# Optimization experiments

Measured on AMD Instinct MI355X. Metric: run time of the kernel, lower is better.

## Reference

```python
import jax, jax.numpy as jnp
import numpy as np

N_AGENTS = 32
N_HEADS = 8
HEAD_DIM = 32          # atten_dim // n_heads
HID = 256              # rnn_hidden_dim
ATT = 256              # atten_dim
N_ACT = 32
NEG = -1e9             # finite stand-in for -inf; exp underflows to 0 in softmax


def setup_inputs() -> dict:
    key = jax.random.key(0)
    ks = jax.random.split(key, 20)
    B, N, E = 4096, 64, 128
    w = lambda k, shape: (jax.random.normal(k, shape, jnp.float32) * 0.05)
    return {
        "inputs": jax.random.normal(ks[0], (B, N, E), jnp.float32),
        "hidden_state": jax.random.normal(ks[1], (B, N_AGENTS, HID), jnp.float32) * 0.1,
        "fc1_w": w(ks[2], (HID, E)), "fc1_b": jnp.zeros((HID,), jnp.float32),
        "q_w": w(ks[3], (ATT, HID)), "q_b": jnp.zeros((ATT,), jnp.float32),
        "k_w": w(ks[4], (ATT, HID)), "k_b": jnp.zeros((ATT,), jnp.float32),
        "v_w": w(ks[5], (ATT, HID)), "v_b": jnp.zeros((ATT,), jnp.float32),
        "w_ih": w(ks[6], (3 * HID, ATT)), "w_hh": w(ks[7], (3 * HID, HID)),
        "b_ih": jnp.zeros((3 * HID,), jnp.float32), "b_hh": jnp.zeros((3 * HID,), jnp.float32),
        "out_w": w(ks[8], (N_ACT, HID)), "out_b": jnp.zeros((N_ACT,), jnp.float32),
        "obs_mask": jax.random.randint(ks[9], (B, N, N), 0, 2).astype(bool),
        "scenario_mask": jax.random.randint(ks[10], (B, N_AGENTS), 0, 2).astype(bool),
    }


def reference(inputs, hidden_state, fc1_w, fc1_b, q_w, q_b, k_w, k_b, v_w, v_b,
              w_ih, w_hh, b_ih, b_hh, out_w, out_b, obs_mask, scenario_mask):
    B, N, _ = inputs.shape
    A, nh, e = N_AGENTS, N_HEADS, HEAD_DIM
    # fc1 + ReLU: [B, N, HID]
    x = jax.nn.relu(inputs @ fc1_w.T + fc1_b)
    # multi-head projections; queries only for the first A entities (agents)
    q = (x[:, :A] @ q_w.T + q_b).reshape(B, A, nh, e).transpose(0, 2, 1, 3)   # [B,nh,A,e]
    k = (x @ k_w.T + k_b).reshape(B, N, nh, e).transpose(0, 2, 3, 1)          # [B,nh,e,N]
    v = jax.nn.relu(x @ v_w.T + v_b).reshape(B, N, nh, e).transpose(0, 2, 1, 3)  # [B,nh,N,e]
    score = jnp.einsum('bhae,bhen->bhan', q, k) / np.float32(np.sqrt(e))      # [B,nh,A,N]
    m = obs_mask[:, :A, :][:, None, :, :]                                      # [B,1,A,N]
    score = jnp.where(m, NEG, score)
    w = jax.nn.softmax(score, axis=-1)
    # original: fully-masked rows give NaN then are zeroed; here zero all masked slots
    w = jnp.where(m, 0.0, w)
    att = jnp.einsum('bhan,bhne->bhae', w, v)                                  # [B,nh,A,e]
    att = att.transpose(0, 2, 1, 3).reshape(B * A, nh * e)                     # [B*A, ATT]
    # GRUCell step (PyTorch gate ordering: r, z, n)
    h0 = hidden_state.reshape(B * A, HID)
    gi = att @ w_ih.T + b_ih
    gh = h0 @ w_hh.T + b_hh
    ir, iz, in_ = jnp.split(gi, 3, axis=-1)
    hr, hz, hn = jnp.split(gh, 3, axis=-1)
    r = jax.nn.sigmoid(ir + hr)
    z = jax.nn.sigmoid(iz + hz)
    n = jnp.tanh(in_ + r * hn)
    h = (1.0 - z) * n + z * h0
    h = h.reshape(B, A, HID)
    am = scenario_mask[:, :, None]                                             # [B,A,1]
    h = jnp.where(am, 0.0, h)
    q_out = h @ out_w.T + out_b
    q_out = jnp.where(am, 0.0, q_out)
    return q_out, h
```

## Files before the change

kernel.cpp:

```cpp
#include <hip/hip_runtime.h>


using bfrag = __attribute__((ext_vector_type(8))) short;
using ffrag = __attribute__((ext_vector_type(4))) float;

#define MFMA(a,b,c) __builtin_amdgcn_mfma_f32_16x16x32_bf16((a),(b),(c),0,0,0)
#define SWZ(row,col,S,xm) ((row)*(S) + ((((col)&~7) ^ (((row)&(xm))<<3)) | ((col)&7)))

#define OFF_A2   0L
#define OFF_FC1  67108864L
#define OFF_QW   67141632L
#define OFF_KW   67207168L
#define OFF_VW   67272704L
#define OFF_WIH  67338240L
#define OFF_WHH  67534848L
#define OFF_OW   67731456L
#define OFF_FLAG 67739648L
#define WS_NEED_BYTES 135479552L

__device__ inline unsigned short f2bf(float x){
  union { float f; unsigned u; } v; v.f = x;
  unsigned r = v.u + 0x7fffu + ((v.u >> 16) & 1u);
  return (unsigned short)(r >> 16);
}
__device__ inline float bf2f(short b){
  union { unsigned u; float f; } v; v.u = ((unsigned)(unsigned short)b) << 16;
  return v.f;
}
__device__ inline bool getmask(const void* p, long i, int byteflag){
  return byteflag ? (((const unsigned char*)p)[i] != 0)
                  : (((const int*)p)[i] != 0);
}
__device__ inline ffrag fzero(){ ffrag z; z[0]=0.f; z[1]=0.f; z[2]=0.f; z[3]=0.f; return z; }
__device__ inline void gload16(const short* g, short* l){
  __builtin_amdgcn_global_load_lds((const __attribute__((address_space(1))) void*)g,
                                   (__attribute__((address_space(3))) void*)l, 16, 0, 0);
}

__global__ void k0_prep(const float* __restrict__ fc1, const float* __restrict__ qw,
    const float* __restrict__ kw, const float* __restrict__ vw, const float* __restrict__ wih,
    const float* __restrict__ whh, const float* __restrict__ ow, const float* __restrict__ h0,
    const void* __restrict__ obsm, short* __restrict__ ws){
  long tid = (long)blockIdx.x*blockDim.x + threadIdx.x;
  long n = (long)gridDim.x*blockDim.x;
  if (tid == 0){
    const int* mi = (const int*)obsm;
    int f = 0;
    for (int i=0;i<256;i++){ if ((unsigned)mi[i] > 1u){ f = 1; break; } }
    ((int*)(ws + OFF_FLAG))[0] = f;
  }
  for (long i=tid; i<32768; i+=n) ws[OFF_FC1+i] = (short)f2bf(fc1[i]);
  for (long i=tid; i<65536; i+=n){
    ws[OFF_QW+i] = (short)f2bf(qw[i]);
    ws[OFF_KW+i] = (short)f2bf(kw[i]);
    ws[OFF_VW+i] = (short)f2bf(vw[i]);
  }
  for (long i=tid; i<196608; i+=n){
    int R = (int)(i >> 8), c = (int)(i & 255);
    int gate = R >> 8, grow = R & 255;
    int jb = grow >> 5, row = grow & 31;
    long dst = (long)((jb*3 + gate)*32 + row)*256 + (c ^ ((row&7)<<3));
    ws[OFF_WIH + dst] = (short)f2bf(wih[i]);
    ws[OFF_WHH + dst] = (short)f2bf(whh[i]);
  }
  for (long i=tid; i<8192; i+=n) ws[OFF_OW+i] = (short)f2bf(ow[i]);
  const float2* h2 = (const float2*)h0;
  unsigned* a2u = (unsigned*)(ws + OFF_A2);
  for (long i=tid; i<16777216L; i+=n){
    long row = i >> 7; int j = (int)(i & 127);
    float2 v = h2[i];
    unsigned pk = (unsigned)f2bf(v.x) | ((unsigned)f2bf(v.y) << 16);
    a2u[row*256 + 128 + j] = pk;
  }
}

__global__ __launch_bounds__(512) void k1_fqkv(const float* __restrict__ inp,
    const short* __restrict__ fc1B, const float* __restrict__ fc1_b,
    const short* __restrict__ wq, const short* __restrict__ wk, const short* __restrict__ wv,
    const float* __restrict__ qb, const float* __restrict__ kb, const float* __restrict__ vb,
    short* __restrict__ A2, short* __restrict__ kC, short* __restrict__ vC, int chunkB){
  __shared__ __align__(16) short smem[65536];
  short* a_s  = smem;
  short* fw_s = smem + 16384;
  short* x_s  = smem;
  int t = threadIdx.x;
  long R0 = (long)blockIdx.x * 128;
  long grow0 = (long)chunkB*131072 + R0;
  int lane = t&63, w = t>>6, lr = lane&15, ko = lane>>4;
  for (int i=0;i<4;i++){
    int c = t + i*512; int row = c>>4; int cc = (c&15)*8;
    const float* src = inp + (grow0 + row)*128 + cc;
    float4 f0 = *(const float4*)src; float4 f1 = *(const float4*)(src+4);
    bfrag v8;
    v8[0]=(short)f2bf(f0.x); v8[1]=(short)f2bf(f0.y); v8[2]=(short)f2bf(f0.z); v8[3]=(short)f2bf(f0.w);
    v8[4]=(short)f2bf(f1.x); v8[5]=(short)f2bf(f1.y); v8[6]=(short)f2bf(f1.z); v8[7]=(short)f2bf(f1.w);
    *(bfrag*)(a_s + SWZ(row, cc, 128, 7)) = v8;
  }
  for (int i=0;i<8;i++){
    int c = t + i*512; int row = c>>4; int cc = (c&15)*8;
    *(bfrag*)(fw_s + SWZ(row, cc, 128, 7)) = *(const bfrag*)(fc1B + row*128 + cc);
  }
  __syncthreads();
  ffrag acc1[16];
  #pragma unroll
  for (int i=0;i<16;i++) acc1[i]=fzero();
  for (int ks=0; ks<4; ks++){
    int kc = ks*32 + ko*8;
    bfrag a = *(const bfrag*)(a_s + SWZ(w*16+lr, kc, 128, 7));
    #pragma unroll
    for (int nt=0; nt<16; nt++){
      bfrag bb = *(const bfrag*)(fw_s + SWZ(nt*16+lr, kc, 128, 7));
      acc1[nt] = MFMA(a, bb, acc1[nt]);
    }
  }
  __syncthreads();
  #pragma unroll
  for (int nt=0; nt<16; nt++){
    float bias = fc1_b[nt*16+lr];
    #pragma unroll
    for (int r=0;r<4;r++){
      int row = w*16 + ko*4 + r;
      float v = acc1[nt][r] + bias; v = v>0.f?v:0.f;
      x_s[SWZ(row, nt*16+lr, 256, 7)] = (short)f2bf(v);
    }
  }
  bfrag a_r[8];
  #pragma unroll
  for (int ks=0; ks<8; ks++)
    a_r[ks] = *(const bfrag*)(x_s + SWZ(w*16+lr, ks*32+ko*8, 256, 7));
  auto STAGE2 = [&](int s){
    int kind = s>>2; int rb = (s&3)*64;
    const short* wsrc = (kind==0?wq:(kind==1?wk:wv)) + (long)rb*256;
    short* dst = smem + 32768 + (s&1)*16384;
    #pragma unroll
    for (int i=0;i<4;i++){
      int c = t + i*512; int row = c>>5; int cc = (c&31)*8;
      *(bfrag*)(dst + SWZ(row, cc, 256, 7)) = *(const bfrag*)(wsrc + (long)row*256 + cc);
    }
  };
  STAGE2(0);
  __syncthreads();
  for (int s=0; s<12; s++){
    if (s < 11) STAGE2(s+1);
    const short* wcur = smem + 32768 + (s&1)*16384;
    ffrag acc2[4];
    #pragma unroll
    for (int i=0;i<4;i++) acc2[i]=fzero();
    #pragma unroll
    for (int ks=0; ks<8; ks++){
      int kc = ks*32 + ko*8;
      #pragma unroll
      for (int nt=0; nt<4; nt++){
        bfrag bb = *(const bfrag*)(wcur + SWZ(nt*16+lr, kc, 256, 7));
        acc2[nt] = MFMA(a_r[ks], bb, acc2[nt]);
      }
    }
    int kind = s>>2; int rb = (s&3)*64;
    const float* bsrc = (kind==0?qb:(kind==1?kb:vb));
    #pragma unroll
    for (int nt=0; nt<4; nt++){
      int colk = rb + nt*16 + lr;
      float bias = bsrc[colk];
      #pragma unroll
      for (int r=0;r<4;r++){
        int row = w*16 + ko*4 + r;
        long rl = R0 + row;
        float v = acc2[nt][r] + bias;
        if (kind==0){
          if ((row&32)==0){
            long grow = grow0 + row;
            long qrow = ((grow>>6)<<5) + (grow&31);
            A2[qrow*512 + colk] = (short)f2bf(v);
          }
        } else if (kind==1){
          kC[rl*256 + colk] = (short)f2bf(v);
        } else {
          v = v>0.f?v:0.f;
          vC[rl*256 + colk] = (short)f2bf(v);
        }
      }
    }
    __syncthreads();
  }
}

__global__ __launch_bounds__(512,4) void k2_attn(const short* __restrict__ kC,
    const short* __restrict__ vC, const void* __restrict__ obsm, short* __restrict__ A2,
    const int* __restrict__ flagp, int chunkB){
  __shared__ __align__(16) short vT_s[8][2048];
  __shared__ __align__(16) short p_s[8][2048];
  __shared__ unsigned char m_s[2048];
  int t = threadIdx.x, bl = blockIdx.x;
  long b = (long)chunkB*2048 + bl;
  int lane = t&63, w = t>>6, lr = lane&15, ko = lane>>4;
  int mflag = *flagp;
  if (mflag){
    uchar4 mv = *(const uchar4*)((const unsigned char*)obsm + b*4096 + t*4);
    m_s[t*4]=mv.x; m_s[t*4+1]=mv.y; m_s[t*4+2]=mv.z; m_s[t*4+3]=mv.w;
  } else {
    int4 mv = *(const int4*)((const int*)obsm + b*4096 + t*4);
    m_s[t*4]  =(unsigned char)(mv.x!=0); m_s[t*4+1]=(unsigned char)(mv.y!=0);
    m_s[t*4+2]=(unsigned char)(mv.z!=0); m_s[t*4+3]=(unsigned char)(mv.w!=0);
  }
  const int h = w;
  const short* qh = A2 + ((long)b*32)*512 + h*32 + ko*8;
  bfrag a_q[2];
  #pragma unroll
  for (int mt=0; mt<2; mt++) a_q[mt] = *(const bfrag*)(qh + (long)(mt*16+lr)*512);
  const short* kh = kC + ((long)bl*64)*256 + h*32 + ko*8;
  bfrag b_k[4];
  #pragma unroll
  for (int nt=0; nt<4; nt++) b_k[nt] = *(const bfrag*)(kh + (nt*16+lr)*256);
  #pragma unroll
  for (int i=0;i<4;i++){
    int n = i*16 + (lane>>2); int e0 = (lane&3)*8;
    bfrag vv = *(const bfrag*)(vC + ((long)bl*64 + n)*256 + h*32 + e0);
    #pragma unroll
    for (int j=0;j<8;j++) vT_s[w][SWZ(e0+j, n, 64, 7)] = vv[j];
  }
  ffrag sc[2][4];
  #pragma unroll
  for (int mt=0; mt<2; mt++)
    #pragma unroll
    for (int nt=0; nt<4; nt++) sc[mt][nt] = MFMA(a_q[mt], b_k[nt], fzero());
  __syncthreads();
  const float scale = 0.17677669529663687f;
  float rsi[2][4];
  #pragma unroll
  for (int mt=0; mt<2; mt++){
    #pragma unroll
    for (int r=0; r<4; r++){
      int arow = mt*16 + ko*4 + r;
      float sv[4]; int mk[4];
      #pragma unroll
      for (int nt=0; nt<4; nt++){
        mk[nt] = m_s[arow*64 + nt*16 + lr];
        sv[nt] = sc[mt][nt][r] * scale;
      }
      float mx = -3.0e38f;
      #pragma unroll
      for (int nt=0; nt<4; nt++) if (!mk[nt]) mx = fmaxf(mx, sv[nt]);
      for (int d=1; d<16; d<<=1) mx = fmaxf(mx, __shfl_xor(mx, d));
      float sum = 0.f;
      #pragma unroll
      for (int nt=0; nt<4; nt++){
        float p = mk[nt] ? 0.f : __expf(sv[nt]-mx);
        sv[nt] = p; sum += p;
      }
      for (int d=1; d<16; d<<=1) sum += __shfl_xor(sum, d);
      rsi[mt][r] = sum > 0.f ? 1.f/sum : 0.f;
      #pragma unroll
      for (int nt=0; nt<4; nt++)
        p_s[w][SWZ(arow, nt*16+lr, 64, 7)] = (short)f2bf(sv[nt]);
    }
  }
  ffrag o[2][2];
  #pragma unroll
  for (int mt=0;mt<2;mt++)
    #pragma unroll
    for (int nt=0;nt<2;nt++) o[mt][nt]=fzero();
  #pragma unroll
  for (int kk=0; kk<2; kk++){
    int kc = kk*32 + ko*8;
    bfrag pa0 = *(const bfrag*)(p_s[w]  + SWZ(lr,    kc, 64, 7));
    bfrag pa1 = *(const bfrag*)(p_s[w]  + SWZ(16+lr, kc, 64, 7));
    bfrag bv0 = *(const bfrag*)(vT_s[w] + SWZ(lr,    kc, 64, 7));
    bfrag bv1 = *(const bfrag*)(vT_s[w] + SWZ(16+lr, kc, 64, 7));
    o[0][0]=MFMA(pa0,bv0,o[0][0]); o[0][1]=MFMA(pa0,bv1,o[0][1]);
    o[1][0]=MFMA(pa1,bv0,o[1][0]); o[1][1]=MFMA(pa1,bv1,o[1][1]);
  }
  #pragma unroll
  for (int mt=0; mt<2; mt++)
    #pragma unroll
    for (int nt=0; nt<2; nt++)
      #pragma unroll
      for (int r=0; r<4; r++){
        int a = mt*16 + ko*4 + r;
        A2[((long)b*32 + a)*512 + h*32 + nt*16 + lr] = (short)f2bf(o[mt][nt][r]*rsi[mt][r]);
      }
}

__global__ __launch_bounds__(512) void k3_gru(const short* __restrict__ A2,
    const short* __restrict__ wihS, const short* __restrict__ whhS,
    const float* __restrict__ b_ih, const float* __restrict__ b_hh,
    const void* __restrict__ scen, float* __restrict__ hout, const int* __restrict__ flagp){
  __shared__ __align__(16) short w_s[2][24576];
  int t = threadIdx.x, bid = blockIdx.x;
  long R0 = (long)bid * 128;
  int mflag = *flagp;
  int lane = t&63, w = t>>6, lr = lane&15, ko = lane>>4;
  long rowbase = R0 + (long)w*16;
  auto STAGE = [&](int jb, int part){
    const short* src = (part ? whhS : wihS) + (long)jb*24576;
    short* dst = w_s[part];
    #pragma unroll
    for (int i=0;i<6;i++)
      gload16(src + (long)(i*512 + t)*8, dst + (i*512 + (t & ~63))*8);
  };
  STAGE(0,0);
  const short* Ab = A2 + (rowbase + lr)*512 + ko*8;
  bfrag A[16];
  #pragma unroll
  for (int ks=0; ks<16; ks++)
    A[ks] = *(const bfrag*)(Ab + ks*32);
  __syncthreads();
  for (int jb=0; jb<8; jb++){
    ffrag aR[2], aZ[2], aI[2], aN[2];
    #pragma unroll
    for (int nt=0;nt<2;nt++){ aR[nt]=fzero(); aZ[nt]=fzero(); aI[nt]=fzero(); aN[nt]=fzero(); }
    STAGE(jb,1);
    {
      const short* wc = w_s[0];
      #pragma unroll
      for (int ks=0; ks<8; ks++){
        int kc = ks*32 + ko*8;
        #pragma unroll
        for (int nt=0; nt<2; nt++){
          bfrag bR = *(const bfrag*)(wc + 0*8192 + SWZ(nt*16+lr, kc, 256, 7));
          aR[nt] = MFMA(A[ks], bR, aR[nt]);
          bfrag bZ = *(const bfrag*)(wc + 1*8192 + SWZ(nt*16+lr, kc, 256, 7));
          aZ[nt] = MFMA(A[ks], bZ, aZ[nt]);
          bfrag bX = *(const bfrag*)(wc + 2*8192 + SWZ(nt*16+lr, kc, 256, 7));
          aI[nt] = MFMA(A[ks], bX, aI[nt]);
        }
      }
    }
    __syncthreads();
    if (jb < 7) STAGE(jb+1,0);
    {
      const short* wc = w_s[1];
      #pragma unroll
      for (int ks=0; ks<8; ks++){
        int kc = ks*32 + ko*8;
        #pragma unroll
        for (int nt=0; nt<2; nt++){
          bfrag bR = *(const bfrag*)(wc + 0*8192 + SWZ(nt*16+lr, kc, 256, 7));
          aR[nt] = MFMA(A[8+ks], bR, aR[nt]);
          bfrag bZ = *(const bfrag*)(wc + 1*8192 + SWZ(nt*16+lr, kc, 256, 7));
          aZ[nt] = MFMA(A[8+ks], bZ, aZ[nt]);
          bfrag bX = *(const bfrag*)(wc + 2*8192 + SWZ(nt*16+lr, kc, 256, 7));
          aN[nt] = MFMA(A[8+ks], bX, aN[nt]);
        }
      }
    }
    #pragma unroll
    for (int nt=0; nt<2; nt++){
      int j = jb*32 + nt*16 + lr;
      float bir = b_ih[j],     bhr = b_hh[j];
      float biz = b_ih[256+j], bhz = b_hh[256+j];
      float bin = b_ih[512+j], bhn = b_hh[512+j];
      #pragma unroll
      for (int rr=0; rr<4; rr++){
        long row = rowbase + ko*4 + rr;
        float rg = 1.f/(1.f + __expf(-(aR[nt][rr] + bir + bhr)));
        float zg = 1.f/(1.f + __expf(-(aZ[nt][rr] + biz + bhz)));
        float ag = aI[nt][rr] + bin + rg*(aN[nt][rr] + bhn);
        float ng = 2.f/(1.f + __expf(-2.f*ag)) - 1.f;
        float h0v = bf2f(A2[row*512 + 256 + j]);
        float hv = (1.f - zg)*ng + zg*h0v;
        if (getmask(scen, row, mflag)) hv = 0.f;
        hout[row*256 + j] = hv;
      }
    }
    __syncthreads();
  }
}

__global__ __launch_bounds__(512) void k4_out(const float* __restrict__ hout,
    const short* __restrict__ ow, const float* __restrict__ out_b,
    const void* __restrict__ scen, float* __restrict__ qout, const int* __restrict__ flagp){
  __shared__ __align__(16) short ow_s[32*256];
  int t = threadIdx.x; long R0 = (long)blockIdx.x * 256;
  int mflag = *flagp;
  for (int i=0;i<2;i++){
    int c = t + i*512; int row = c >> 5; int cc = (c & 31)*8;
    *(bfrag*)(ow_s + SWZ(row, cc, 256, 7)) = *(const bfrag*)(ow + row*256 + cc);
  }
  __syncthreads();
  int lane = t&63, w = t>>6, lr = lane&15, ko = lane>>4;
  ffrag acc[2][2];
  #pragma unroll
  for (int a=0;a<2;a++) for (int bq=0;bq<2;bq++) acc[a][bq]=fzero();
  for (int ks=0; ks<8; ks++){
    int kc = ks*32 + ko*8;
    #pragma unroll
    for (int mi=0; mi<2; mi++){
      long row = R0 + (w*2+mi)*16 + lr;
      const float* hp = hout + row*256 + kc;
      float4 f0 = *(const float4*)hp; float4 f1 = *(const float4*)(hp+4);
      bfrag a;
      a[0]=(short)f2bf(f0.x); a[1]=(short)f2bf(f0.y); a[2]=(short)f2bf(f0.z); a[3]=(short)f2bf(f0.w);
      a[4]=(short)f2bf(f1.x); a[5]=(short)f2bf(f1.y); a[6]=(short)f2bf(f1.z); a[7]=(short)f2bf(f1.w);
      #pragma unroll
      for (int nt=0; nt<2; nt++){
        bfrag bb = *(const bfrag*)(ow_s + SWZ(nt*16+lr, kc, 256, 7));
        acc[mi][nt] = MFMA(a, bb, acc[mi][nt]);
      }
    }
  }
  #pragma unroll
  for (int mi=0;mi<2;mi++)
    #pragma unroll
    for (int nt=0;nt<2;nt++){
      int col = nt*16 + lr;
      float ob = out_b[col];
      #pragma unroll
      for (int r=0;r<4;r++){
        long row = R0 + (w*2+mi)*16 + ko*4 + r;
        float qv = acc[mi][nt][r] + ob;
        if (getmask(scen, row, mflag)) qv = 0.f;
        qout[row*32 + col] = qv;
      }
    }
}

extern "C" void kernel_launch(void* const* d_in, const int* in_sizes, int n_in,
                              void* d_out, int out_size, void* d_ws, size_t ws_size,
                              hipStream_t stream){
  const float* inputs = (const float*)d_in[0];
  const float* hidden = (const float*)d_in[1];
  const float* fc1_w  = (const float*)d_in[2];
  const float* fc1_b  = (const float*)d_in[3];
  const float* q_w    = (const float*)d_in[4];
  const float* q_b    = (const float*)d_in[5];
  const float* k_w    = (const float*)d_in[6];
  const float* k_b    = (const float*)d_in[7];
  const float* v_w    = (const float*)d_in[8];
  const float* v_b    = (const float*)d_in[9];
  const float* w_ih   = (const float*)d_in[10];
  const float* w_hh   = (const float*)d_in[11];
  const float* b_ih   = (const float*)d_in[12];
  const float* b_hh   = (const float*)d_in[13];
  const float* out_w  = (const float*)d_in[14];
  const float* out_b  = (const float*)d_in[15];
  const void* obsm    = d_in[16];
  const void* scen    = d_in[17];
  (void)in_sizes; (void)n_in; (void)out_size;
  if ((long)ws_size < WS_NEED_BYTES) return;
  short* ws = (short*)d_ws;
  const int* flagp = (const int*)(ws + OFF_FLAG);
  float* qout = (float*)d_out;
  float* hout = qout + 4194304;
  short* kCs = (short*)hout;
  short* vCs = kCs + 33554432L;
  short* A2  = ws + OFF_A2;

  hipLaunchKernelGGL(k0_prep, dim3(2048), dim3(256), 0, stream,
      fc1_w, q_w, k_w, v_w, w_ih, w_hh, out_w, hidden, obsm, ws);
  for (int c=0; c<2; c++){
    hipLaunchKernelGGL(k1_fqkv, dim3(1024), dim3(512), 0, stream,
        inputs, ws + OFF_FC1, fc1_b, ws + OFF_QW, ws + OFF_KW, ws + OFF_VW,
        q_b, k_b, v_b, A2, kCs, vCs, c);
    hipLaunchKernelGGL(k2_attn, dim3(2048), dim3(512), 0, stream,
        kCs, vCs, obsm, A2, flagp, c);
  }
  hipLaunchKernelGGL(k3_gru, dim3(1024), dim3(512), 0, stream,
      A2, ws + OFF_WIH, ws + OFF_WHH, b_ih, b_hh, scen, hout, flagp);
  hipLaunchKernelGGL(k4_out, dim3(512), dim3(512), 0, stream,
      hout, ws + OFF_OW, out_b, scen, qout, flagp);
}
```

Baseline: 612.8 us.

## Restage GRU weights into 32 KB phases to shrink LDS and deepen pipelining

Measured after the change: 612.5 us. Within noise of the previous version (-0.0%).

```diff
diff --git a/kernel.cpp b/kernel.cpp
--- a/kernel.cpp
+++ b/kernel.cpp
@@ -12,8 +12,7 @@
 #define OFF_QW   67141632L
 #define OFF_KW   67207168L
 #define OFF_VW   67272704L
-#define OFF_WIH  67338240L
-#define OFF_WHH  67534848L
+#define OFF_W6   67338240L
 #define OFF_OW   67731456L
 #define OFF_FLAG 67739648L
 #define WS_NEED_BYTES 135479552L
@@ -56,12 +55,13 @@
     ws[OFF_VW+i] = (short)f2bf(vw[i]);
   }
   for (long i=tid; i<196608; i+=n){
-    int R = (int)(i >> 8), c = (int)(i & 255);
-    int gate = R >> 8, grow = R & 255;
+    int gate = (int)(i >> 16);
+    int grow = (int)((i >> 8) & 255);
+    int c = (int)(i & 255);
     int jb = grow >> 5, row = grow & 31;
-    long dst = (long)((jb*3 + gate)*32 + row)*256 + (c ^ ((row&7)<<3));
-    ws[OFF_WIH + dst] = (short)f2bf(wih[i]);
-    ws[OFF_WHH + dst] = (short)f2bf(whh[i]);
+    int cs = c ^ ((row&7)<<3);
+    ws[OFF_W6 + ((long)((jb*6 + gate)*32 + row))*256 + cs]     = (short)f2bf(wih[i]);
+    ws[OFF_W6 + ((long)((jb*6 + 3 + gate)*32 + row))*256 + cs] = (short)f2bf(whh[i]);
   }
   for (long i=tid; i<8192; i+=n) ws[OFF_OW+i] = (short)f2bf(ow[i]);
   const float2* h2 = (const float2*)h0;
@@ -281,23 +281,22 @@
 }
 
 __global__ __launch_bounds__(512) void k3_gru(const short* __restrict__ A2,
-    const short* __restrict__ wihS, const short* __restrict__ whhS,
-    const float* __restrict__ b_ih, const float* __restrict__ b_hh,
+    const short* __restrict__ w6, const float* __restrict__ b_ih, const float* __restrict__ b_hh,
     const void* __restrict__ scen, float* __restrict__ hout, const int* __restrict__ flagp){
-  __shared__ __align__(16) short w_s[2][24576];
+  __shared__ __align__(16) short w_s[2][16384];
   int t = threadIdx.x, bid = blockIdx.x;
   long R0 = (long)bid * 128;
   int mflag = *flagp;
   int lane = t&63, w = t>>6, lr = lane&15, ko = lane>>4;
   long rowbase = R0 + (long)w*16;
-  auto STAGE = [&](int jb, int part){
-    const short* src = (part ? whhS : wihS) + (long)jb*24576;
-    short* dst = w_s[part];
-    #pragma unroll
-    for (int i=0;i<6;i++)
+  auto STAGE = [&](int ph){
+    const short* src = w6 + (long)ph*16384;
+    short* dst = w_s[ph&1];
+    #pragma unroll
+    for (int i=0;i<4;i++)
       gload16(src + (long)(i*512 + t)*8, dst + (i*512 + (t & ~63))*8);
   };
-  STAGE(0,0);
+  STAGE(0);
   const short* Ab = A2 + (rowbase + lr)*512 + ko*8;
   bfrag A[16];
   #pragma unroll
@@ -308,61 +307,53 @@
     ffrag aR[2], aZ[2], aI[2], aN[2];
     #pragma unroll
     for (int nt=0;nt<2;nt++){ aR[nt]=fzero(); aZ[nt]=fzero(); aI[nt]=fzero(); aN[nt]=fzero(); }
-    STAGE(jb,1);
-    {
-      const short* wc = w_s[0];
+    #pragma unroll
+    for (int p=0; p<3; p++){
+      int ph = jb*3 + p;
+      if (ph < 23) STAGE(ph+1);
+      const short* wc = w_s[ph&1];
       #pragma unroll
       for (int ks=0; ks<8; ks++){
         int kc = ks*32 + ko*8;
         #pragma unroll
         for (int nt=0; nt<2; nt++){
-          bfrag bR = *(const bfrag*)(wc + 0*8192 + SWZ(nt*16+lr, kc, 256, 7));
-          aR[nt] = MFMA(A[ks], bR, aR[nt]);
-          bfrag bZ = *(const bfrag*)(wc + 1*8192 + SWZ(nt*16+lr, kc, 256, 7));
-          aZ[nt] = MFMA(A[ks], bZ, aZ[nt]);
-          bfrag bX = *(const bfrag*)(wc + 2*8192 + SWZ(nt*16+lr, kc, 256, 7));
-          aI[nt] = MFMA(A[ks], bX, aI[nt]);
+          bfrag b0 = *(const bfrag*)(wc + SWZ(nt*16+lr, kc, 256, 7));
+          bfrag b1 = *(const bfrag*)(wc + 8192 + SWZ(nt*16+lr, kc, 256, 7));
+          if (p == 0){
+            aR[nt] = MFMA(A[ks], b0, aR[nt]);
+            aZ[nt] = MFMA(A[ks], b1, aZ[nt]);
+          } else if (p == 1){
+            aI[nt] = MFMA(A[ks], b0, aI[nt]);
+            aR[nt] = MFMA(A[8+ks], b1, aR[nt]);
+          } else {
+            aZ[nt] = MFMA(A[8+ks], b0, aZ[nt]);
+            aN[nt] = MFMA(A[8+ks], b1, aN[nt]);
+          }
         }
       }
-    }
-    __syncthreads();
-    if (jb < 7) STAGE(jb+1,0);
-    {
-      const short* wc = w_s[1];
-      #pragma unroll
-      for (int ks=0; ks<8; ks++){
-        int kc = ks*32 + ko*8;
+      if (p == 2){
         #pragma unroll
         for (int nt=0; nt<2; nt++){
-          bfrag bR = *(const bfrag*)(wc + 0*8192 + SWZ(nt*16+lr, kc, 256, 7));
-          aR[nt] = MFMA(A[8+ks], bR, aR[nt]);
-          bfrag bZ = *(const bfrag*)(wc + 1*8192 + SWZ(nt*16+lr, kc, 256, 7));
-          aZ[nt] = MFMA(A[8+ks], bZ, aZ[nt]);
-          bfrag bX = *(const bfrag*)(wc + 2*8192 + SWZ(nt*16+lr, kc, 256, 7));
-          aN[nt] = MFMA(A[8+ks], bX, aN[nt]);
+          int j = jb*32 + nt*16 + lr;
+          float bir = b_ih[j],     bhr = b_hh[j];
+          float biz = b_ih[256+j], bhz = b_hh[256+j];
+          float bin = b_ih[512+j], bhn = b_hh[512+j];
+          #pragma unroll
+          for (int rr=0; rr<4; rr++){
+            long row = rowbase + ko*4 + rr;
+            float rg = 1.f/(1.f + __expf(-(aR[nt][rr] + bir + bhr)));
+            float zg = 1.f/(1.f + __expf(-(aZ[nt][rr] + biz + bhz)));
+            float ag = aI[nt][rr] + bin + rg*(aN[nt][rr] + bhn);
+            float ng = 2.f/(1.f + __expf(-2.f*ag)) - 1.f;
+            float h0v = bf2f(A2[row*512 + 256 + j]);
+            float hv = (1.f - zg)*ng + zg*h0v;
+            if (getmask(scen, row, mflag)) hv = 0.f;
+            hout[row*256 + j] = hv;
+          }
         }
       }
-    }
-    #pragma unroll
-    for (int nt=0; nt<2; nt++){
-      int j = jb*32 + nt*16 + lr;
-      float bir = b_ih[j],     bhr = b_hh[j];
-      float biz = b_ih[256+j], bhz = b_hh[256+j];
-      float bin = b_ih[512+j], bhn = b_hh[512+j];
-      #pragma unroll
-      for (int rr=0; rr<4; rr++){
-        long row = rowbase + ko*4 + rr;
-        float rg = 1.f/(1.f + __expf(-(aR[nt][rr] + bir + bhr)));
-        float zg = 1.f/(1.f + __expf(-(aZ[nt][rr] + biz + bhz)));
-        float ag = aI[nt][rr] + bin + rg*(aN[nt][rr] + bhn);
-        float ng = 2.f/(1.f + __expf(-2.f*ag)) - 1.f;
-        float h0v = bf2f(A2[row*512 + 256 + j]);
-        float hv = (1.f - zg)*ng + zg*h0v;
-        if (getmask(scen, row, mflag)) hv = 0.f;
-        hout[row*256 + j] = hv;
-      }
-    }
-    __syncthreads();
+      __syncthreads();
+    }
   }
 }
 
@@ -455,7 +446,7 @@
         kCs, vCs, obsm, A2, flagp, c);
   }
   hipLaunchKernelGGL(k3_gru, dim3(1024), dim3(512), 0, stream,
-      A2, ws + OFF_WIH, ws + OFF_WHH, b_ih, b_hh, scen, hout, flagp);
+      A2, ws + OFF_W6, b_ih, b_hh, scen, hout, flagp);
   hipLaunchKernelGGL(k4_out, dim3(512), dim3(512), 0, stream,
       hout, ws + OFF_OW, out_b, scen, qout, flagp);
 }
```
